# Performance work log

Hardware: AMD Instinct MI355X
Metric: run time of the kernel (lower is better)

## Reference

```python
import jax, jax.numpy as jnp
import numpy as np

EPS = 1e-08


def _l2norm(x):
    return x / (jnp.linalg.norm(x, axis=-1, keepdims=True) + EPS)


def _mlp(x, weights):
    # weights: list of (W, b); gelu between layers, none after last
    n = len(weights)
    for i, (W, b) in enumerate(weights):
        x = x @ W + b
        if i < n - 1:
            x = jax.nn.gelu(x)  # approximate gelu, matches jax.nn.gelu default
    return x


def setup_inputs() -> dict:
    key = jax.random.key(0)
    ks = jax.random.split(key, 16)
    N, A, L, K = 65536, 32, 256, 1024
    enc_dims = [A, 512, 1024, L]
    dec_dims = [L, 1024, 512, A]

    def lin(k, din, dout):
        kw, kb = jax.random.split(k)
        W = jax.random.normal(kw, (din, dout), jnp.float32) / np.sqrt(din)
        b = jnp.zeros((dout,), jnp.float32)
        return W, b

    inp = {}
    inp["action"] = jax.random.normal(ks[0], (N, A), jnp.float32)
    inp["dim_weights"] = jax.random.uniform(ks[1], (A,), jnp.float32)
    for i in range(3):
        W, b = lin(ks[2 + i], enc_dims[i], enc_dims[i + 1])
        inp[f"enc_w{i}"], inp[f"enc_b{i}"] = W, b
    for i in range(3):
        W, b = lin(ks[5 + i], dec_dims[i], dec_dims[i + 1])
        inp[f"dec_w{i}"], inp[f"dec_b{i}"] = W, b
    cb = jax.random.normal(ks[8], (K, L), jnp.float32) * 0.1
    inp["codebook"] = _l2norm(cb)
    return inp


def reference(action, dim_weights,
              enc_w0, enc_b0, enc_w1, enc_b1, enc_w2, enc_b2,
              dec_w0, dec_b0, dec_w1, dec_b1, dec_w2, dec_b2,
              codebook):
    enc = [(enc_w0, enc_b0), (enc_w1, enc_b1), (enc_w2, enc_b2)]
    dec = [(dec_w0, dec_b0), (dec_w1, dec_b1), (dec_w2, dec_b2)]

    z_e = _l2norm(_mlp(action, enc))                       # [N, L]
    cb = _l2norm(codebook)                                 # [K, L]
    # squared euclidean distances [N, K]
    dists = (jnp.sum(z_e * z_e, axis=-1, keepdims=True)
             - 2.0 * z_e @ cb.T
             + jnp.sum(cb * cb, axis=-1))
    code_idx = jnp.argmin(dists, axis=-1)                  # [N]
    z_q = cb[code_idx]                                     # [N, L]

    z_q_ste = z_e + jax.lax.stop_gradient(z_q - z_e)
    action_hat = _mlp(z_q_ste, dec)                        # [N, A]

    sq_err = (action - action_hat) ** 2 * dim_weights
    recon_loss = jnp.mean(sq_err)
    codebook_loss = jnp.mean((jax.lax.stop_gradient(z_e) - z_q) ** 2)
    commit_loss = jnp.mean((z_e - jax.lax.stop_gradient(z_q)) ** 2)
    return action_hat, code_idx, recon_loss, codebook_loss, commit_loss
```

## Files before the change

### kernel.cpp

```cpp
#include <hip/hip_runtime.h>
#include <math.h>

#define N_ROWS 65536

typedef short short8 __attribute__((ext_vector_type(8)));
typedef float f32x4 __attribute__((ext_vector_type(4)));

__device__ __forceinline__ float gelu_f(float x) {
  float x3 = x * x * x;
  float t = tanhf(0.7978845608028654f * (x + 0.044715f * x3));
  return 0.5f * x * (1.0f + t);
}

__device__ __forceinline__ unsigned short f2bf(float f) {
  unsigned u = __float_as_uint(f);
  unsigned r = u + 0x7fffu + ((u >> 16) & 1u);
  return (unsigned short)(r >> 16);
}
__device__ __forceinline__ float bf2f(unsigned short h) {
  return __uint_as_float(((unsigned)h) << 16);
}

__device__ __forceinline__ void split3(float v, unsigned short& p0,
                                       unsigned short& p1, unsigned short& p2) {
  p0 = f2bf(v);
  float r = v - bf2f(p0);
  p1 = f2bf(r);
  r -= bf2f(p1);
  p2 = f2bf(r);
}

__device__ __forceinline__ void split3f(float v, unsigned short& p0,
                                        unsigned short& p1, unsigned short& p2) {
  unsigned u = __float_as_uint(v);
  unsigned h0 = (u + 0x8000u) & 0xffff0000u;
  float r = v - __uint_as_float(h0);
  unsigned u1 = __float_as_uint(r);
  unsigned h1 = (u1 + 0x8000u) & 0xffff0000u;
  float r2 = r - __uint_as_float(h1);
  p0 = (unsigned short)(h0 >> 16);
  p1 = (unsigned short)(h1 >> 16);
  p2 = f2bf(r2);
}

__device__ __forceinline__ void split2f(float v, unsigned short& p0,
                                        unsigned short& p1) {
  unsigned u = __float_as_uint(v);
  unsigned h0 = (u + 0x8000u) & 0xffff0000u;
  float r = v - __uint_as_float(h0);
  p0 = (unsigned short)(h0 >> 16);
  p1 = f2bf(r);
}

__device__ __forceinline__ f32x4 mfma16(short8 a, short8 b, f32x4 c) {
  return __builtin_amdgcn_mfma_f32_16x16x32_bf16(a, b, c, 0, 0, 0);
}

__global__ __launch_bounds__(256) void gemm_enc0_split(
    const float* __restrict__ A, const float* __restrict__ W,
    const float* __restrict__ bias, unsigned short* __restrict__ P,
    size_t aps, int din, int dout) {
  __shared__ float As[16][132];
  __shared__ float Ws[16][132];
  int t = threadIdx.x;
  int tx = t & 15, ty = t >> 4;
  int c0 = blockIdx.x * 128;
  int r0 = blockIdx.y * 128;

  float acc[8][8];
#pragma unroll
  for (int i = 0; i < 8; ++i)
#pragma unroll
    for (int j = 0; j < 8; ++j) acc[i][j] = 0.0f;

  int kchunks = din >> 4;
  for (int kc = 0; kc < kchunks; ++kc) {
    int k0 = kc << 4;
    __syncthreads();
#pragma unroll
    for (int it = 0; it < 2; ++it) {
      int id = t + it * 256;
      int r = id >> 2;
      int kq = (id & 3) * 4;
      float4 v = *(const float4*)&A[(long)(r0 + r) * din + (k0 + kq)];
      As[kq + 0][r] = v.x; As[kq + 1][r] = v.y;
      As[kq + 2][r] = v.z; As[kq + 3][r] = v.w;
      int k = id >> 5;
      int cq = (id & 31) * 4;
      float4 w = *(const float4*)&W[(long)(k0 + k) * dout + (c0 + cq)];
      *(float4*)&Ws[k][cq] = w;
    }
    __syncthreads();
#pragma unroll
    for (int k = 0; k < 16; ++k) {
      float av[8], bv[8];
      *(float4*)&av[0] = *(const float4*)&As[k][ty * 4];
      *(float4*)&av[4] = *(const float4*)&As[k][ty * 4 + 64];
      *(float4*)&bv[0] = *(const float4*)&Ws[k][tx * 4];
      *(float4*)&bv[4] = *(const float4*)&Ws[k][tx * 4 + 64];
#pragma unroll
      for (int i = 0; i < 8; ++i)
#pragma unroll
        for (int j = 0; j < 8; ++j)
          acc[i][j] = fmaf(av[i], bv[j], acc[i][j]);
    }
  }

  float bbv[8];
  *(float4*)&bbv[0] = *(const float4*)&bias[c0 + tx * 4];
  *(float4*)&bbv[4] = *(const float4*)&bias[c0 + tx * 4 + 64];
#pragma unroll
  for (int i = 0; i < 8; ++i) {
    long row = r0 + ty * 4 + (i & 3) + ((i >> 2) * 64);
    unsigned short s0[8], s1[8], s2[8];
#pragma unroll
    for (int j = 0; j < 8; ++j) {
      float v = gelu_f(acc[i][j] + bbv[j]);
      split3f(v, s0[j], s1[j], s2[j]);
    }
    size_t b = (size_t)row * dout + c0 + tx * 4;
    ushort4 w;
    w.x = s0[0]; w.y = s0[1]; w.z = s0[2]; w.w = s0[3];
    *(ushort4*)&P[b] = w;
    w.x = s0[4]; w.y = s0[5]; w.z = s0[6]; w.w = s0[7];
    *(ushort4*)&P[b + 64] = w;
    w.x = s1[0]; w.y = s1[1]; w.z = s1[2]; w.w = s1[3];
    *(ushort4*)&P[aps + b] = w;
    w.x = s1[4]; w.y = s1[5]; w.z = s1[6]; w.w = s1[7];
    *(ushort4*)&P[aps + b + 64] = w;
    w.x = s2[0]; w.y = s2[1]; w.z = s2[2]; w.w = s2[3];
    *(ushort4*)&P[2 * aps + b] = w;
    w.x = s2[4]; w.y = s2[5]; w.z = s2[6]; w.w = s2[7];
    *(ushort4*)&P[2 * aps + b + 64] = w;
  }
}

template <bool GELU>
__global__ __launch_bounds__(256) void gemm64_kernel(
    const float* __restrict__ A, const float* __restrict__ W,
    const float* __restrict__ bias, float* __restrict__ C,
    int din, int dout) {
  __shared__ float As[16][68];
  __shared__ float Ws[16][68];
  int t = threadIdx.x;
  int tx = t & 15, ty = t >> 4;
  int c0 = blockIdx.x * 64;
  int r0 = blockIdx.y * 64;

  float acc[4][4];
#pragma unroll
  for (int i = 0; i < 4; ++i)
#pragma unroll
    for (int j = 0; j < 4; ++j) acc[i][j] = 0.0f;

  int kchunks = din >> 4;
  for (int kc = 0; kc < kchunks; ++kc) {
    int k0 = kc << 4;
    __syncthreads();
    {
      int r = t >> 2, kq = (t & 3) * 4;
      float4 v = *(const float4*)&A[(long)(r0 + r) * din + (k0 + kq)];
      As[kq + 0][r] = v.x; As[kq + 1][r] = v.y;
      As[kq + 2][r] = v.z; As[kq + 3][r] = v.w;
      int k = t >> 4, cq = (t & 15) * 4;
      *(float4*)&Ws[k][cq] = *(const float4*)&W[(long)(k0 + k) * dout + (c0 + cq)];
    }
    __syncthreads();
#pragma unroll
    for (int k = 0; k < 16; ++k) {
      float av[4], bv[4];
      *(float4*)&av[0] = *(const float4*)&As[k][ty * 4];
      *(float4*)&bv[0] = *(const float4*)&Ws[k][tx * 4];
#pragma unroll
      for (int i = 0; i < 4; ++i)
#pragma unroll
        for (int j = 0; j < 4; ++j)
          acc[i][j] = fmaf(av[i], bv[j], acc[i][j]);
    }
  }

  float4 bb = *(const float4*)&bias[c0 + tx * 4];
#pragma unroll
  for (int i = 0; i < 4; ++i) {
    long row = r0 + ty * 4 + i;
    float o[4];
    o[0] = acc[i][0] + bb.x; o[1] = acc[i][1] + bb.y;
    o[2] = acc[i][2] + bb.z; o[3] = acc[i][3] + bb.w;
    if (GELU) {
      o[0] = gelu_f(o[0]); o[1] = gelu_f(o[1]);
      o[2] = gelu_f(o[2]); o[3] = gelu_f(o[3]);
    }
    *(float4*)&C[row * dout + c0 + tx * 4] = *(float4*)&o[0];
  }
}

__global__ void frag_pack_kernel(const float* __restrict__ W,
                                 unsigned short* __restrict__ Bf,
                                 int K, int N) {
  int l = threadIdx.x;
  int m = l & 15, q = l >> 4;
  int cb = blockIdx.x, kb = blockIdx.y;
  unsigned short s0[8], s1[8], s2[8];
#pragma unroll
  for (int j = 0; j < 8; ++j) {
    float v = W[(long)(kb * 32 + q * 8 + j) * N + cb * 16 + m];
    split3(v, s0[j], s1[j], s2[j]);
  }
  size_t base = ((size_t)cb * (K / 32) + kb) * 3 * 512;
  *(short8*)&Bf[base + 0 * 512 + l * 8] = *(short8*)s0;
  *(short8*)&Bf[base + 1 * 512 + l * 8] = *(short8*)s1;
  *(short8*)&Bf[base + 2 * 512 + l * 8] = *(short8*)s2;
}

__global__ void frag_pack2_t(const float* __restrict__ cbn,
                             unsigned short* __restrict__ Bf) {
  int l = threadIdx.x;
  int m = l & 15, q = l >> 4;
  int cb = blockIdx.x, kb = blockIdx.y;
  unsigned short s0[8], s1[8];
  const float* src = cbn + (long)(cb * 16 + m) * 256 + kb * 32 + q * 8;
#pragma unroll
  for (int j = 0; j < 8; ++j) split2f(src[j], s0[j], s1[j]);
  size_t base = ((size_t)(cb * 8 + kb) * 2) * 512;
  *(short8*)&Bf[base + l * 8] = *(short8*)s0;
  *(short8*)&Bf[base + 512 + l * 8] = *(short8*)s1;
}

template <bool GELU>
__global__ __launch_bounds__(256) void mfma3_gemm(
    const unsigned short* __restrict__ Ap, size_t aps,
    const unsigned short* __restrict__ Bf,
    const float* __restrict__ bias, float* __restrict__ C,
    int K, int dout) {
  __shared__ unsigned short A_f[3 * 2 * 4 * 512];
  int t = threadIdx.x;
  int lane = t & 63, wave = t >> 6;
  int q = lane >> 4, m = lane & 15;
  int wrb = wave >> 1;
  int wr = wrb * 64, wc = (wave & 1) * 64;

  int gx = gridDim.x, tot = gx * gridDim.y;
  int lin = blockIdx.y * gx + blockIdx.x;
  if (!(tot & 7)) lin = (lin & 7) * (tot >> 3) + (lin >> 3);
  int bx = lin % gx, by = lin / gx;

  long r0 = (long)by * 128;
  int c0 = bx * 128;
  int kchunks = K >> 5;

  f32x4 acc[4][4];
#pragma unroll
  for (int i = 0; i < 4; ++i)
#pragma unroll
    for (int j = 0; j < 4; ++j) acc[i][j] = (f32x4){0.f, 0.f, 0.f, 0.f};

  int rs = t >> 1, hs = (t & 1) * 16;
  const unsigned short* a0p = Ap + (size_t)(r0 + rs) * K + hs;
  const unsigned short* a1p = a0p + aps;
  const unsigned short* a2p = a0p + 2 * aps;
  int cb0 = (c0 + wc) >> 4;
  int xw = (rs >> 4) & 3, wrbw = rs >> 6, mw = rs & 15;
  int g0 = ((t & 1) * 2 + 0) * 16 + mw;
  int g1 = ((t & 1) * 2 + 1) * 16 + mw;
  int wb0 = (0 * 2 + wrbw) * 4 + xw;
  int wb1 = (1 * 2 + wrbw) * 4 + xw;
  int wb2 = (2 * 2 + wrbw) * 4 + xw;

  for (int kb = 0; kb < kchunks; ++kb) {
    __syncthreads();
    {
      int kt = kb << 5;
      uint4 u00 = *(const uint4*)(a0p + kt);
      uint4 u01 = *(const uint4*)(a0p + kt + 8);
      uint4 u10 = *(const uint4*)(a1p + kt);
      uint4 u11 = *(const uint4*)(a1p + kt + 8);
      uint4 u20 = *(const uint4*)(a2p + kt);
      uint4 u21 = *(const uint4*)(a2p + kt + 8);
      *(uint4*)&A_f[wb0 * 512 + g0 * 8] = u00;
      *(uint4*)&A_f[wb0 * 512 + g1 * 8] = u01;
      *(uint4*)&A_f[wb1 * 512 + g0 * 8] = u10;
      *(uint4*)&A_f[wb1 * 512 + g1 * 8] = u11;
      *(uint4*)&A_f[wb2 * 512 + g0 * 8] = u20;
      *(uint4*)&A_f[wb2 * 512 + g1 * 8] = u21;
    }
    __syncthreads();
    short8 af[3][4];
#pragma unroll
    for (int p = 0; p < 3; ++p)
#pragma unroll
      for (int x = 0; x < 4; ++x)
        af[p][x] = *(const short8*)&A_f[((p * 2 + wrb) * 4 + x) * 512 + lane * 8];
#pragma unroll
    for (int ct = 0; ct < 4; ++ct) {
      size_t fb = ((size_t)(cb0 + ct) * kchunks + kb) * 3 * 512 + lane * 8;
      short8 b0 = *(const short8*)&Bf[fb];
      short8 b1 = *(const short8*)&Bf[fb + 512];
      short8 b2 = *(const short8*)&Bf[fb + 1024];
#pragma unroll
      for (int rt = 0; rt < 4; ++rt) {
        acc[rt][ct] = mfma16(af[0][rt], b0, acc[rt][ct]);
        acc[rt][ct] = mfma16(af[0][rt], b1, acc[rt][ct]);
        acc[rt][ct] = mfma16(af[1][rt], b0, acc[rt][ct]);
        acc[rt][ct] = mfma16(af[0][rt], b2, acc[rt][ct]);
        acc[rt][ct] = mfma16(af[1][rt], b1, acc[rt][ct]);
        acc[rt][ct] = mfma16(af[2][rt], b0, acc[rt][ct]);
      }
    }
  }

#pragma unroll
  for (int ct = 0; ct < 4; ++ct) {
    long col = c0 + wc + ct * 16 + m;
    float bv = bias[col];
#pragma unroll
    for (int rt = 0; rt < 4; ++rt) {
      long rowb = r0 + wr + rt * 16 + q * 4;
#pragma unroll
      for (int r = 0; r < 4; ++r) {
        float v = acc[rt][ct][r] + bv;
        if (GELU) v = gelu_f(v);
        C[(rowb + r) * dout + col] = v;
      }
    }
  }
}

__global__ __launch_bounds__(256) void mfma3_norm(
    const float* __restrict__ A, const unsigned short* __restrict__ Bf,
    const float* __restrict__ bias, float* __restrict__ z_e,
    float* __restrict__ ze2) {
  __shared__ unsigned short A_f[3 * 4 * 512];
  __shared__ float S[64][4];
  __shared__ float Sinv[64];
  const int K = 1024, kchunks = 32;
  int t = threadIdx.x;
  int lane = t & 63, wave = t >> 6;
  int q = lane >> 4, m = lane & 15;
  long r0 = (long)blockIdx.x * 64;

  f32x4 acc[4][4];
#pragma unroll
  for (int i = 0; i < 4; ++i)
#pragma unroll
    for (int j = 0; j < 4; ++j) acc[i][j] = (f32x4){0.f, 0.f, 0.f, 0.f};

  int rs = t >> 2, kq = t & 3;
  const float* aptr = A + (r0 + rs) * K + kq * 8;
  int xw = rs >> 4, mw = rs & 15;
  int gw = kq * 16 + mw;
  int wb0 = 0 * 4 + xw, wb1 = 1 * 4 + xw, wb2 = 2 * 4 + xw;
  int cb0 = wave * 4;

  for (int kb = 0; kb < kchunks; ++kb) {
    __syncthreads();
    {
      float fv[8];
      *(float4*)&fv[0] = *(const float4*)(aptr + (kb << 5));
      *(float4*)&fv[4] = *(const float4*)(aptr + (kb << 5) + 4);
      unsigned short a0[8], a1[8], a2[8];
#pragma unroll
      for (int i = 0; i < 8; ++i) split3f(fv[i], a0[i], a1[i], a2[i]);
      *(uint4*)&A_f[wb0 * 512 + gw * 8] = *(uint4*)a0;
      *(uint4*)&A_f[wb1 * 512 + gw * 8] = *(uint4*)a1;
      *(uint4*)&A_f[wb2 * 512 + gw * 8] = *(uint4*)a2;
    }
    __syncthreads();
    short8 af[3][4];
#pragma unroll
    for (int p = 0; p < 3; ++p)
#pragma unroll
      for (int x = 0; x < 4; ++x)
        af[p][x] = *(const short8*)&A_f[(p * 4 + x) * 512 + lane * 8];
#pragma unroll
    for (int ct = 0; ct < 4; ++ct) {
      size_t fb = ((size_t)(cb0 + ct) * kchunks + kb) * 3 * 512 + lane * 8;
      short8 b0 = *(const short8*)&Bf[fb];
      short8 b1 = *(const short8*)&Bf[fb + 512];
      short8 b2 = *(const short8*)&Bf[fb + 1024];
#pragma unroll
      for (int rt = 0; rt < 4; ++rt) {
        acc[rt][ct] = mfma16(af[0][rt], b0, acc[rt][ct]);
        acc[rt][ct] = mfma16(af[0][rt], b1, acc[rt][ct]);
        acc[rt][ct] = mfma16(af[1][rt], b0, acc[rt][ct]);
        acc[rt][ct] = mfma16(af[0][rt], b2, acc[rt][ct]);
        acc[rt][ct] = mfma16(af[1][rt], b1, acc[rt][ct]);
        acc[rt][ct] = mfma16(af[2][rt], b0, acc[rt][ct]);
      }
    }
  }

#pragma unroll
  for (int ct = 0; ct < 4; ++ct) {
    float bv = bias[wave * 64 + ct * 16 + m];
#pragma unroll
    for (int rt = 0; rt < 4; ++rt)
#pragma unroll
      for (int r = 0; r < 4; ++r) acc[rt][ct][r] += bv;
  }

#pragma unroll
  for (int rt = 0; rt < 4; ++rt)
#pragma unroll
    for (int r = 0; r < 4; ++r) {
      float s = acc[rt][0][r] * acc[rt][0][r] + acc[rt][1][r] * acc[rt][1][r] +
                acc[rt][2][r] * acc[rt][2][r] + acc[rt][3][r] * acc[rt][3][r];
#pragma unroll
      for (int off = 1; off <= 8; off <<= 1) s += __shfl_xor(s, off);
      if (m == 0) S[rt * 16 + q * 4 + r][wave] = s;
    }
  __syncthreads();
  if (t < 64) {
    float s = S[t][0] + S[t][1] + S[t][2] + S[t][3];
    float den = sqrtf(s) + 1e-8f;
    Sinv[t] = 1.0f / den;
    ze2[r0 + t] = s / (den * den);
  }
  __syncthreads();
#pragma unroll
  for (int rt = 0; rt < 4; ++rt)
#pragma unroll
    for (int r = 0; r < 4; ++r) {
      int rl = rt * 16 + q * 4 + r;
      float inv = Sinv[rl];
#pragma unroll
      for (int ct = 0; ct < 4; ++ct)
        z_e[(r0 + rl) * 256 + wave * 64 + ct * 16 + m] = acc[rt][ct][r] * inv;
    }
}

__global__ __launch_bounds__(256) void dist2_mfma(
    const float* __restrict__ z_e, const unsigned short* __restrict__ cbf,
    int* __restrict__ idxc, int* __restrict__ fixcnt, int* __restrict__ fixlist) {
  __shared__ unsigned short A_f[2 * 8 * 4 * 512];
  __shared__ float Lv1[64][4], Lv2[64][4];
  __shared__ int Lc1[64][4];
  int t = threadIdx.x;
  int lane = t & 63, wave = t >> 6;
  int q = lane >> 4, m = lane & 15;
  long r0 = (long)blockIdx.x * 64;

#pragma unroll
  for (int it = 0; it < 4; ++it) {
    int kb = it * 2 + (t >> 7);
    int rs = (t & 127) >> 1, hs = (t & 1) * 16;
    const float* ap = z_e + (r0 + rs) * 256 + kb * 32 + hs;
    float fv[16];
    *(float4*)&fv[0] = *(const float4*)(ap + 0);
    *(float4*)&fv[4] = *(const float4*)(ap + 4);
    *(float4*)&fv[8] = *(const float4*)(ap + 8);
    *(float4*)&fv[12] = *(const float4*)(ap + 12);
    unsigned short a0[16], a1[16];
#pragma unroll
    for (int i = 0; i < 16; ++i) split2f(fv[i], a0[i], a1[i]);
    int x = rs >> 4, mm = rs & 15;
    int ga = ((t & 1) * 2 + 0) * 16 + mm;
    int gb = ((t & 1) * 2 + 1) * 16 + mm;
    int b0 = ((0 * 8 + kb) * 4 + x) * 512;
    int b1 = ((1 * 8 + kb) * 4 + x) * 512;
    *(uint4*)&A_f[b0 + ga * 8] = ((uint4*)a0)[0];
    *(uint4*)&A_f[b0 + gb * 8] = ((uint4*)a0)[1];
    *(uint4*)&A_f[b1 + ga * 8] = ((uint4*)a1)[0];
    *(uint4*)&A_f[b1 + gb * 8] = ((uint4*)a1)[1];
  }
  __syncthreads();

  float v1[4][4], v2[4][4];
  int c1[4][4];
#pragma unroll
  for (int i = 0; i < 4; ++i)
#pragma unroll
    for (int j = 0; j < 4; ++j) { v1[i][j] = -3.4e38f; v2[i][j] = -3.4e38f; c1[i][j] = 0; }

  for (int ctp = 0; ctp < 4; ++ctp) {
    f32x4 acc[4][4];
#pragma unroll
    for (int i = 0; i < 4; ++i)
#pragma unroll
      for (int j = 0; j < 4; ++j) acc[i][j] = (f32x4){0.f, 0.f, 0.f, 0.f};

    for (int kb = 0; kb < 8; ++kb) {
      short8 af0[4], af1[4];
#pragma unroll
      for (int rt = 0; rt < 4; ++rt) {
        af0[rt] = *(const short8*)&A_f[((0 * 8 + kb) * 4 + rt) * 512 + lane * 8];
        af1[rt] = *(const short8*)&A_f[((1 * 8 + kb) * 4 + rt) * 512 + lane * 8];
      }
      short8 bf0[4], bf1[4];
#pragma unroll
      for (int cs = 0; cs < 4; ++cs) {
        int cb = ctp * 16 + (cs >> 1) * 8 + wave * 2 + (cs & 1);
        size_t fb = ((size_t)(cb * 8 + kb) * 2) * 512 + lane * 8;
        bf0[cs] = *(const short8*)&cbf[fb];
        bf1[cs] = *(const short8*)&cbf[fb + 512];
      }
#pragma unroll
      for (int rt = 0; rt < 4; ++rt)
#pragma unroll
        for (int cs = 0; cs < 4; ++cs) {
          acc[rt][cs] = mfma16(af0[rt], bf0[cs], acc[rt][cs]);
          acc[rt][cs] = mfma16(af0[rt], bf1[cs], acc[rt][cs]);
          acc[rt][cs] = mfma16(af1[rt], bf0[cs], acc[rt][cs]);
        }
    }
#pragma unroll
    for (int rt = 0; rt < 4; ++rt)
#pragma unroll
      for (int cs = 0; cs < 4; ++cs) {
        int colb = ctp * 256 + (cs >> 1) * 128 + wave * 32 + (cs & 1) * 16 + m;
#pragma unroll
        for (int r = 0; r < 4; ++r) {
          float v = acc[rt][cs][r];
          float nv2 = fmaxf(v2[rt][r], fminf(v, v1[rt][r]));
          if (v > v1[rt][r]) { c1[rt][r] = colb; v1[rt][r] = v; }
          v2[rt][r] = nv2;
        }
      }
  }

#pragma unroll
  for (int off = 1; off <= 8; off <<= 1) {
#pragma unroll
    for (int rt = 0; rt < 4; ++rt)
#pragma unroll
      for (int r = 0; r < 4; ++r) {
        float ov1 = __shfl_xor(v1[rt][r], off);
        float ov2 = __shfl_xor(v2[rt][r], off);
        int oc1 = __shfl_xor(c1[rt][r], off);
        float nv2 = fmaxf(fmaxf(v2[rt][r], ov2), fminf(v1[rt][r], ov1));
        if (ov1 > v1[rt][r] || (ov1 == v1[rt][r] && oc1 < c1[rt][r])) {
          v1[rt][r] = ov1; c1[rt][r] = oc1;
        }
        v2[rt][r] = nv2;
      }
  }
  if (m == 0) {
#pragma unroll
    for (int rt = 0; rt < 4; ++rt)
#pragma unroll
      for (int r = 0; r < 4; ++r) {
        int rloc = rt * 16 + q * 4 + r;
        Lv1[rloc][wave] = v1[rt][r];
        Lv2[rloc][wave] = v2[rt][r];
        Lc1[rloc][wave] = c1[rt][r];
      }
  }
  __syncthreads();
  if (t < 64) {
    float a1 = Lv1[t][0], a2 = Lv2[t][0];
    int ac = Lc1[t][0];
#pragma unroll
    for (int w = 1; w < 4; ++w) {
      float b1 = Lv1[t][w], b2 = Lv2[t][w];
      int bc = Lc1[t][w];
      float n2 = fmaxf(fmaxf(a2, b2), fminf(a1, b1));
      if (b1 > a1 || (b1 == a1 && bc < ac)) { a1 = b1; ac = bc; }
      a2 = n2;
    }
    idxc[r0 + t] = ac;
    if (a1 - a2 < 5.0e-4f) {
      int p = atomicAdd(fixcnt, 1);
      fixlist[p] = r0 + t;
    }
  }
}

__global__ __launch_bounds__(256) void fixup_part(
    const float* __restrict__ z_e, const float* __restrict__ cbn,
    const float* __restrict__ ze2, const float* __restrict__ cb2,
    const int* __restrict__ fixlist, const int* __restrict__ fixcnt,
    float* __restrict__ fixbv, int* __restrict__ fixbc) {
  int cnt = *fixcnt;
  int r0 = blockIdx.y * 128;
  if (r0 >= cnt) return;
  int ctile = blockIdx.x;
  int c0 = ctile * 128;
  __shared__ float As[16][132];
  __shared__ float Ws[16][132];
  __shared__ float rv[128][17];
  __shared__ int rc[128][17];
  __shared__ int rows_l[128];
  int t = threadIdx.x, tx = t & 15, ty = t >> 4;

  if (t < 128) rows_l[t] = fixlist[(r0 + t < cnt) ? (r0 + t) : 0];
  __syncthreads();

  float bestv[8];
  int bestc[8];
  float myze2[8];
#pragma unroll
  for (int i = 0; i < 8; ++i) {
    bestv[i] = 3.4e38f;
    bestc[i] = 0;
    int rl = ty * 4 + (i & 3) + ((i >> 2) * 64);
    myze2[i] = ze2[rows_l[rl]];
  }

  float acc[8][8];
#pragma unroll
  for (int i = 0; i < 8; ++i)
#pragma unroll
    for (int j = 0; j < 8; ++j) acc[i][j] = 0.0f;

  for (int kc = 0; kc < 16; ++kc) {
    int k0 = kc << 4;
    __syncthreads();
#pragma unroll
    for (int it = 0; it < 2; ++it) {
      int id = t + it * 256;
      int r = id >> 2;
      int kq = (id & 3) * 4;
      float4 v = *(const float4*)&z_e[(long)rows_l[r] * 256 + k0 + kq];
      As[kq + 0][r] = v.x; As[kq + 1][r] = v.y;
      As[kq + 2][r] = v.z; As[kq + 3][r] = v.w;
      float4 w = *(const float4*)&cbn[(long)(c0 + r) * 256 + k0 + kq];
      Ws[kq + 0][r] = w.x; Ws[kq + 1][r] = w.y;
      Ws[kq + 2][r] = w.z; Ws[kq + 3][r] = w.w;
    }
    __syncthreads();
#pragma unroll
    for (int k = 0; k < 16; ++k) {
      float av[8], bv[8];
      *(float4*)&av[0] = *(const float4*)&As[k][ty * 4];
      *(float4*)&av[4] = *(const float4*)&As[k][ty * 4 + 64];
      *(float4*)&bv[0] = *(const float4*)&Ws[k][tx * 4];
      *(float4*)&bv[4] = *(const float4*)&Ws[k][tx * 4 + 64];
#pragma unroll
      for (int i = 0; i < 8; ++i)
#pragma unroll
        for (int j = 0; j < 8; ++j)
          acc[i][j] = fmaf(av[i], bv[j], acc[i][j]);
    }
  }

  float cb2v[8];
  *(float4*)&cb2v[0] = *(const float4*)&cb2[c0 + tx * 4];
  *(float4*)&cb2v[4] = *(const float4*)&cb2[c0 + tx * 4 + 64];
#pragma unroll
  for (int i = 0; i < 8; ++i)
#pragma unroll
    for (int j = 0; j < 8; ++j) {
      int c = c0 + tx * 4 + (j & 3) + ((j >> 2) * 64);
      float d = (myze2[i] - 2.0f * acc[i][j]) + cb2v[j];
      if (d < bestv[i] || (d == bestv[i] && c < bestc[i])) {
        bestv[i] = d;
        bestc[i] = c;
      }
    }

  __syncthreads();
#pragma unroll
  for (int i = 0; i < 8; ++i) {
    int rl = ty * 4 + (i & 3) + ((i >> 2) * 64);
    rv[rl][tx] = bestv[i];
    rc[rl][tx] = bestc[i];
  }
  __syncthreads();
  if (t < 128 && r0 + t < cnt) {
    float bv = rv[t][0];
    int bc = rc[t][0];
    for (int j = 1; j < 16; ++j) {
      float v = rv[t][j];
      int c = rc[t][j];
      if (v < bv || (v == bv && c < bc)) { bv = v; bc = c; }
    }
    fixbv[(long)(r0 + t) * 8 + ctile] = bv;
    fixbc[(long)(r0 + t) * 8 + ctile] = bc;
  }
}

__global__ __launch_bounds__(256) void fixup_reduce(
    const float* __restrict__ fixbv, const int* __restrict__ fixbc,
    const int* __restrict__ fixlist, const int* __restrict__ fixcnt,
    int* __restrict__ idxc) {
  int cnt = *fixcnt;
  int i = blockIdx.x * 256 + threadIdx.x;
  if (i >= cnt) return;
  float bv = fixbv[(long)i * 8];
  int bc = fixbc[(long)i * 8];
#pragma unroll
  for (int j = 1; j < 8; ++j) {
    float v = fixbv[(long)i * 8 + j];
    int c = fixbc[(long)i * 8 + j];
    if (v < bv || (v == bv && c < bc)) { bv = v; bc = c; }
  }
  idxc[fixlist[i]] = bc;
}

__global__ __launch_bounds__(256) void rownorm_kernel(
    const float* __restrict__ in, float* __restrict__ outv,
    float* __restrict__ outsq) {
  int wid = threadIdx.x >> 6, lane = threadIdx.x & 63;
  long row = (long)blockIdx.x * 4 + wid;
  const float* src = in + row * 256;
  float4 v = *(const float4*)&src[lane * 4];
  float s = v.x * v.x + v.y * v.y + v.z * v.z + v.w * v.w;
#pragma unroll
  for (int off = 32; off >= 1; off >>= 1) s += __shfl_xor(s, off);
  float denom = sqrtf(s) + 1e-8f;
  float4 o;
  o.x = v.x / denom; o.y = v.y / denom; o.z = v.z / denom; o.w = v.w / denom;
  *(float4*)&outv[row * 256 + lane * 4] = o;
  float s2 = o.x * o.x + o.y * o.y + o.z * o.z + o.w * o.w;
#pragma unroll
  for (int off = 32; off >= 1; off >>= 1) s2 += __shfl_xor(s2, off);
  if (lane == 0) outsq[row] = s2;
}

__global__ __launch_bounds__(256) void t2_kernel(
    const float* __restrict__ T1, const float* __restrict__ W,
    const float* __restrict__ bias, float* __restrict__ T2) {
  int id = blockIdx.x * 256 + threadIdx.x;
  int row = id >> 5, col = id & 31;
  const float* a = T1 + (long)row * 512;
  float s = 0.f;
#pragma unroll 8
  for (int k = 0; k < 512; ++k) s = fmaf(a[k], W[k * 32 + col], s);
  T2[id] = s + bias[col];
}

__global__ __launch_bounds__(256) void fused_tail(
    const float* __restrict__ z_e, const float* __restrict__ cbn,
    const int* __restrict__ idxc, const float* __restrict__ T2,
    const float* __restrict__ action, const float* __restrict__ dimw,
    float* __restrict__ partRe, float* __restrict__ partCo,
    float* __restrict__ outIdx, float* __restrict__ ahat, int pb) {
  int t = threadIdx.x, wid = t >> 6, lane = t & 63;
  float cs = 0.f, rsum = 0.f;
#pragma unroll
  for (int r = 0; r < 4; ++r) {
    long row = (long)blockIdx.x * 16 + wid * 4 + r;
    int k = idxc[row];
    float4 a = *(const float4*)&z_e[row * 256 + lane * 4];
    float4 b = *(const float4*)&cbn[(long)k * 256 + lane * 4];
    float dx = a.x - b.x, dy = a.y - b.y, dz = a.z - b.z, dq = a.w - b.w;
    cs += dx * dx + dy * dy + dz * dz + dq * dq;
    if (lane < 8) {
      float4 av = *(const float4*)&action[row * 32 + lane * 4];
      float4 tv = *(const float4*)&T2[(long)k * 32 + lane * 4];
      float4 wv = *(const float4*)&dimw[lane * 4];
      *(float4*)&ahat[row * 32 + lane * 4] = tv;
      float ex = av.x - tv.x, ey = av.y - tv.y;
      float ez = av.z - tv.z, ew = av.w - tv.w;
      rsum += ex * ex * wv.x + ey * ey * wv.y + ez * ez * wv.z + ew * ew * wv.w;
    }
    if (lane == 0) outIdx[row] = (float)k;
  }
#pragma unroll
  for (int off = 32; off >= 1; off >>= 1) {
    cs += __shfl_xor(cs, off);
    rsum += __shfl_xor(rsum, off);
  }
  __shared__ float rc[4], rr[4];
  if (lane == 0) { rc[wid] = cs; rr[wid] = rsum; }
  __syncthreads();
  if (t == 0) {
    partCo[pb + blockIdx.x] = rc[0] + rc[1] + rc[2] + rc[3];
    partRe[pb + blockIdx.x] = rr[0] + rr[1] + rr[2] + rr[3];
  }
}

__global__ void zero_kernel(int* __restrict__ cnts) {
  if (threadIdx.x < 32) cnts[threadIdx.x] = 0;
}

__global__ __launch_bounds__(256) void finalize_kernel(
    const float* __restrict__ partRe, const float* __restrict__ partCo,
    float* __restrict__ out) {
  int t = threadIdx.x;
  float sr = 0.f, sc = 0.f;
  for (int i = t; i < 4096; i += 256) { sr += partRe[i]; sc += partCo[i]; }
#pragma unroll
  for (int off = 32; off >= 1; off >>= 1) {
    sr += __shfl_xor(sr, off);
    sc += __shfl_xor(sc, off);
  }
  __shared__ float rs_[4], cs_[4];
  int wid = t >> 6, lane = t & 63;
  if (lane == 0) { rs_[wid] = sr; cs_[wid] = sc; }
  __syncthreads();
  if (t == 0) {
    float r = rs_[0] + rs_[1] + rs_[2] + rs_[3];
    float c = cs_[0] + cs_[1] + cs_[2] + cs_[3];
    out[0] = r / (65536.0f * 32.0f);
    float cl = c / (65536.0f * 256.0f);
    out[1] = cl;
    out[2] = cl;
  }
}

extern "C" void kernel_launch(void* const* d_in, const int* in_sizes, int n_in,
                              void* d_out, int out_size, void* d_ws,
                              size_t ws_size, hipStream_t stream) {
  const float* action = (const float*)d_in[0];
  const float* dimw = (const float*)d_in[1];
  const float* ew0 = (const float*)d_in[2];
  const float* eb0 = (const float*)d_in[3];
  const float* ew1 = (const float*)d_in[4];
  const float* eb1 = (const float*)d_in[5];
  const float* ew2 = (const float*)d_in[6];
  const float* eb2 = (const float*)d_in[7];
  const float* dw0 = (const float*)d_in[8];
  const float* db0 = (const float*)d_in[9];
  const float* dw1 = (const float*)d_in[10];
  const float* db1 = (const float*)d_in[11];
  const float* dw2 = (const float*)d_in[12];
  const float* db2 = (const float*)d_in[13];
  const float* cb = (const float*)d_in[14];
  float* out = (float*)d_out;
  char* ws = (char*)d_ws;

  const size_t fixed_b = 1048576 + 4096 + 1048576 + 3145728 + 1572864 +
                         4194304 + 2097152 + 131072 + 256 + 32768;
  int R = N_ROWS;
  while (R > 2048) {
    if (fixed_b + (size_t)R * 7244 + 65536 <= ws_size) break;
    R >>= 1;
  }

  size_t off = 0;
  float* cbn = (float*)(ws + off); off += 1048576;
  float* cb2 = (float*)(ws + off); off += 4096;
  unsigned short* cbf = (unsigned short*)(ws + off); off += 1048576;
  unsigned short* ewf1 = (unsigned short*)(ws + off); off += 3145728;
  unsigned short* ewf2 = (unsigned short*)(ws + off); off += 1572864;
  float* T0 = (float*)(ws + off); off += 4194304;
  float* T1d = (float*)(ws + off); off += 2097152;
  float* T2d = (float*)(ws + off); off += 131072;
  int* fixcnts = (int*)(ws + off); off += 256;
  float* partRe = (float*)(ws + off); off += 16384;
  float* partCo = (float*)(ws + off); off += 16384;
  float* ze2 = (float*)(ws + off); off += (size_t)R * 4;
  int* idxc = (int*)(ws + off); off += (size_t)R * 4;
  int* fixlist = (int*)(ws + off); off += (size_t)R * 4;
  float* fixbv = (float*)(ws + off); off += (size_t)R * 32;
  int* fixbc = (int*)(ws + off); off += (size_t)R * 32;
  char* P0 = ws + off; off += (size_t)R * 3072;
  char* P1 = ws + off; off += (size_t)R * 4096;

  unsigned short* e0p = (unsigned short*)P0;
  size_t aps0 = (size_t)R * 512;
  float* e1 = (float*)P1;
  float* z_e = (float*)P0;

  zero_kernel<<<1, 64, 0, stream>>>(fixcnts);
  rownorm_kernel<<<256, 256, 0, stream>>>(cb, cbn, cb2);
  frag_pack2_t<<<dim3(64, 8), 64, 0, stream>>>(cbn, cbf);
  frag_pack_kernel<<<dim3(64, 16), 64, 0, stream>>>(ew1, ewf1, 512, 1024);
  frag_pack_kernel<<<dim3(16, 32), 64, 0, stream>>>(ew2, ewf2, 1024, 256);

  gemm64_kernel<true><<<dim3(16, 16), 256, 0, stream>>>(cbn, dw0, db0, T0, 256, 1024);
  gemm64_kernel<true><<<dim3(8, 16), 256, 0, stream>>>(T0, dw1, db1, T1d, 1024, 512);
  t2_kernel<<<128, 256, 0, stream>>>(T1d, dw2, db2, T2d);

  for (int base = 0; base < N_ROWS; base += R) {
    int ci = base / R;
    const float* act_c = action + (size_t)base * 32;
    float* out_c = out + (size_t)base * 32;
    int* fixcnt = &fixcnts[ci];

    gemm_enc0_split<<<dim3(4, R / 128), 256, 0, stream>>>(
        act_c, ew0, eb0, e0p, aps0, 32, 512);
    mfma3_gemm<true><<<dim3(8, R / 128), 256, 0, stream>>>(
        e0p, aps0, ewf1, eb1, e1, 512, 1024);
    mfma3_norm<<<R / 64, 256, 0, stream>>>(e1, ewf2, eb2, z_e, ze2);

    dist2_mfma<<<R / 64, 256, 0, stream>>>(z_e, cbf, idxc, fixcnt, fixlist);
    fixup_part<<<dim3(8, R / 128), 256, 0, stream>>>(
        z_e, cbn, ze2, cb2, fixlist, fixcnt, fixbv, fixbc);
    fixup_reduce<<<R / 256, 256, 0, stream>>>(fixbv, fixbc, fixlist, fixcnt,
                                              idxc);

    fused_tail<<<R / 16, 256, 0, stream>>>(
        z_e, cbn, idxc, T2d, act_c, dimw, partRe, partCo,
        out + 2097152 + base, out_c, base >> 4);
  }

  finalize_kernel<<<1, 256, 0, stream>>>(partRe, partCo, out + 2162688);
}
```

Baseline: 1.155 ms.

## Double-buffer A tiles in LDS for split-bf16 MFMA GEMM kernels

```diff
diff --git a/kernel.cpp b/kernel.cpp
--- a/kernel.cpp
+++ b/kernel.cpp
@@ -232,7 +232,7 @@
     const unsigned short* __restrict__ Bf,
     const float* __restrict__ bias, float* __restrict__ C,
     int K, int dout) {
-  __shared__ unsigned short A_f[3 * 2 * 4 * 512];
+  __shared__ unsigned short A_f[2][3 * 2 * 4 * 512];
   int t = threadIdx.x;
   int lane = t & 63, wave = t >> 6;
   int q = lane >> 4, m = lane & 15;
@@ -266,30 +266,31 @@
   int wb1 = (1 * 2 + wrbw) * 4 + xw;
   int wb2 = (2 * 2 + wrbw) * 4 + xw;
 
+  {
+    uint4 u00 = *(const uint4*)(a0p);
+    uint4 u01 = *(const uint4*)(a0p + 8);
+    uint4 u10 = *(const uint4*)(a1p);
+    uint4 u11 = *(const uint4*)(a1p + 8);
+    uint4 u20 = *(const uint4*)(a2p);
+    uint4 u21 = *(const uint4*)(a2p + 8);
+    *(uint4*)&A_f[0][wb0 * 512 + g0 * 8] = u00;
+    *(uint4*)&A_f[0][wb0 * 512 + g1 * 8] = u01;
+    *(uint4*)&A_f[0][wb1 * 512 + g0 * 8] = u10;
+    *(uint4*)&A_f[0][wb1 * 512 + g1 * 8] = u11;
+    *(uint4*)&A_f[0][wb2 * 512 + g0 * 8] = u20;
+    *(uint4*)&A_f[0][wb2 * 512 + g1 * 8] = u21;
+  }
+  __syncthreads();
+
+  int cur = 0;
   for (int kb = 0; kb < kchunks; ++kb) {
-    __syncthreads();
-    {
-      int kt = kb << 5;
-      uint4 u00 = *(const uint4*)(a0p + kt);
-      uint4 u01 = *(const uint4*)(a0p + kt + 8);
-      uint4 u10 = *(const uint4*)(a1p + kt);
-      uint4 u11 = *(const uint4*)(a1p + kt + 8);
-      uint4 u20 = *(const uint4*)(a2p + kt);
-      uint4 u21 = *(const uint4*)(a2p + kt + 8);
-      *(uint4*)&A_f[wb0 * 512 + g0 * 8] = u00;
-      *(uint4*)&A_f[wb0 * 512 + g1 * 8] = u01;
-      *(uint4*)&A_f[wb1 * 512 + g0 * 8] = u10;
-      *(uint4*)&A_f[wb1 * 512 + g1 * 8] = u11;
-      *(uint4*)&A_f[wb2 * 512 + g0 * 8] = u20;
-      *(uint4*)&A_f[wb2 * 512 + g1 * 8] = u21;
-    }
-    __syncthreads();
     short8 af[3][4];
 #pragma unroll
     for (int p = 0; p < 3; ++p)
 #pragma unroll
       for (int x = 0; x < 4; ++x)
-        af[p][x] = *(const short8*)&A_f[((p * 2 + wrb) * 4 + x) * 512 + lane * 8];
+        af[p][x] =
+            *(const short8*)&A_f[cur][((p * 2 + wrb) * 4 + x) * 512 + lane * 8];
 #pragma unroll
     for (int ct = 0; ct < 4; ++ct) {
       size_t fb = ((size_t)(cb0 + ct) * kchunks + kb) * 3 * 512 + lane * 8;
@@ -306,6 +307,24 @@
         acc[rt][ct] = mfma16(af[2][rt], b0, acc[rt][ct]);
       }
     }
+    if (kb + 1 < kchunks) {
+      int kt = (kb + 1) << 5;
+      uint4 u00 = *(const uint4*)(a0p + kt);
+      uint4 u01 = *(const uint4*)(a0p + kt + 8);
+      uint4 u10 = *(const uint4*)(a1p + kt);
+      uint4 u11 = *(const uint4*)(a1p + kt + 8);
+      uint4 u20 = *(const uint4*)(a2p + kt);
+      uint4 u21 = *(const uint4*)(a2p + kt + 8);
+      int nb = cur ^ 1;
+      *(uint4*)&A_f[nb][wb0 * 512 + g0 * 8] = u00;
+      *(uint4*)&A_f[nb][wb0 * 512 + g1 * 8] = u01;
+      *(uint4*)&A_f[nb][wb1 * 512 + g0 * 8] = u10;
+      *(uint4*)&A_f[nb][wb1 * 512 + g1 * 8] = u11;
+      *(uint4*)&A_f[nb][wb2 * 512 + g0 * 8] = u20;
+      *(uint4*)&A_f[nb][wb2 * 512 + g1 * 8] = u21;
+    }
+    __syncthreads();
+    cur ^= 1;
   }
 
 #pragma unroll
@@ -329,7 +348,7 @@
     const float* __restrict__ A, const unsigned short* __restrict__ Bf,
     const float* __restrict__ bias, float* __restrict__ z_e,
     float* __restrict__ ze2) {
-  __shared__ unsigned short A_f[3 * 4 * 512];
+  __shared__ unsigned short A_f[2][3 * 4 * 512];
   __shared__ float S[64][4];
   __shared__ float Sinv[64];
   const int K = 1024, kchunks = 32;
@@ -351,26 +370,27 @@
   int wb0 = 0 * 4 + xw, wb1 = 1 * 4 + xw, wb2 = 2 * 4 + xw;
   int cb0 = wave * 4;
 
+  {
+    float fv[8];
+    *(float4*)&fv[0] = *(const float4*)(aptr);
+    *(float4*)&fv[4] = *(const float4*)(aptr + 4);
+    unsigned short a0[8], a1[8], a2[8];
+#pragma unroll
+    for (int i = 0; i < 8; ++i) split3f(fv[i], a0[i], a1[i], a2[i]);
+    *(uint4*)&A_f[0][wb0 * 512 + gw * 8] = *(uint4*)a0;
+    *(uint4*)&A_f[0][wb1 * 512 + gw * 8] = *(uint4*)a1;
+    *(uint4*)&A_f[0][wb2 * 512 + gw * 8] = *(uint4*)a2;
+  }
+  __syncthreads();
+
+  int cur = 0;
   for (int kb = 0; kb < kchunks; ++kb) {
-    __syncthreads();
-    {
-      float fv[8];
-      *(float4*)&fv[0] = *(const float4*)(aptr + (kb << 5));
-      *(float4*)&fv[4] = *(const float4*)(aptr + (kb << 5) + 4);
-      unsigned short a0[8], a1[8], a2[8];
-#pragma unroll
-      for (int i = 0; i < 8; ++i) split3f(fv[i], a0[i], a1[i], a2[i]);
-      *(uint4*)&A_f[wb0 * 512 + gw * 8] = *(uint4*)a0;
-      *(uint4*)&A_f[wb1 * 512 + gw * 8] = *(uint4*)a1;
-      *(uint4*)&A_f[wb2 * 512 + gw * 8] = *(uint4*)a2;
-    }
-    __syncthreads();
     short8 af[3][4];
 #pragma unroll
     for (int p = 0; p < 3; ++p)
 #pragma unroll
       for (int x = 0; x < 4; ++x)
-        af[p][x] = *(const short8*)&A_f[(p * 4 + x) * 512 + lane * 8];
+        af[p][x] = *(const short8*)&A_f[cur][(p * 4 + x) * 512 + lane * 8];
 #pragma unroll
     for (int ct = 0; ct < 4; ++ct) {
       size_t fb = ((size_t)(cb0 + ct) * kchunks + kb) * 3 * 512 + lane * 8;
@@ -387,6 +407,20 @@
         acc[rt][ct] = mfma16(af[2][rt], b0, acc[rt][ct]);
       }
     }
+    if (kb + 1 < kchunks) {
+      float fv[8];
+      *(float4*)&fv[0] = *(const float4*)(aptr + ((kb + 1) << 5));
+      *(float4*)&fv[4] = *(const float4*)(aptr + ((kb + 1) << 5) + 4);
+      unsigned short a0[8], a1[8], a2[8];
+#pragma unroll
+      for (int i = 0; i < 8; ++i) split3f(fv[i], a0[i], a1[i], a2[i]);
+      int nb = cur ^ 1;
+      *(uint4*)&A_f[nb][wb0 * 512 + gw * 8] = *(uint4*)a0;
+      *(uint4*)&A_f[nb][wb1 * 512 + gw * 8] = *(uint4*)a1;
+      *(uint4*)&A_f[nb][wb2 * 512 + gw * 8] = *(uint4*)a2;
+    }
+    __syncthreads();
+    cur ^= 1;
   }
 
 #pragma unroll
```

After: 1.126 ms. -2.5%, faster.
